# Kernel optimization log

Hardware: AMD Instinct MI355X
Metric: run time of the kernel (lower is better)

Reference implementation:

```python
import jax, jax.numpy as jnp
import numpy as np

DIM_IN = 1024
DIM_Q = 1024
DIM_K = 1024
DIM_V = 1024
HEADS = 16

def setup_inputs() -> dict:
    key = jax.random.key(0)
    ks = jax.random.split(key, 5)
    s = 1.0 / np.sqrt(DIM_IN)
    return {
        "x": jax.random.normal(ks[0], (2, 2048, DIM_IN), dtype=jnp.float32),
        "Wq": jax.random.uniform(ks[1], (DIM_IN, DIM_Q), jnp.float32, -s, s),
        "Wk": jax.random.uniform(ks[2], (DIM_IN, DIM_K), jnp.float32, -s, s),
        "Wv": jax.random.uniform(ks[3], (DIM_IN, DIM_V), jnp.float32, -s, s),
        "Wo": jax.random.uniform(ks[4], (DIM_V, DIM_V), jnp.float32, -1.0/np.sqrt(DIM_V), 1.0/np.sqrt(DIM_V)),
    }

def reference(x, Wq, Wk, Wv, Wo):
    B, S, _ = x.shape
    H = HEADS
    q = (x @ Wq).reshape(B, S, H, DIM_Q // H).transpose(0, 2, 1, 3)  # [B,H,S,dq]
    k = (x @ Wk).reshape(B, S, H, DIM_K // H).transpose(0, 2, 1, 3)
    v = (x @ Wv).reshape(B, S, H, DIM_V // H).transpose(0, 2, 1, 3)
    scores = jnp.einsum("bhsd,bhtd->bhst", q, k)  # no pre-softmax scaling (as in source)
    # NOTE: source divides by sqrt(dim_q) AFTER softmax — replicated faithfully.
    attn = jax.nn.softmax(scores, axis=-1) / jnp.sqrt(jnp.float32(DIM_Q))
    out = jnp.einsum("bhst,bhtd->bhsd", attn, v)  # [B,H,S,dv]
    out = out.transpose(0, 2, 1, 3).reshape(B, S, DIM_V)
    return out @ Wo
```

## Files before the change

### kernel.cpp

```cpp
#include <hip/hip_runtime.h>
#include <hip/hip_bf16.h>


typedef __attribute__((ext_vector_type(8))) short bf16x8;
typedef __attribute__((ext_vector_type(4))) short short4v;
typedef __attribute__((ext_vector_type(4))) float f32x4;
typedef __attribute__((ext_vector_type(2))) unsigned int u32x2;

typedef const __attribute__((address_space(1))) void gvoid_t;
typedef __attribute__((address_space(3))) void svoid_t;
#define GLDS16(g, l) \
  __builtin_amdgcn_global_load_lds((gvoid_t*)(g), (svoid_t*)(l), 16, 0, 0)

#define MFMA16(a, b, c) __builtin_amdgcn_mfma_f32_16x16x32_bf16((a), (b), (c), 0, 0, 0)

#if defined(__has_builtin)
#if __has_builtin(__builtin_amdgcn_exp2f)
#define EXP2(x) __builtin_amdgcn_exp2f(x)
#else
#define EXP2(x) exp2f(x)
#endif
#else
#define EXP2(x) exp2f(x)
#endif

#define LOG2E 1.4426950408889634f
#define NSHIFT 17.312340490667561f

static __device__ __forceinline__ short f2bf(float f) {
  __hip_bfloat16 h = __float2bfloat16(f);
  short s;
  __builtin_memcpy(&s, &h, 2);
  return s;
}

static __device__ __forceinline__ unsigned pack2bf(float lo, float hi) {
  float2 t; t.x = lo; t.y = hi;
  __hip_bfloat162 h2 = __float22bfloat162_rn(t);
  unsigned u;
  __builtin_memcpy(&u, &h2, 4);
  return u;
}

__global__ __launch_bounds__(256) void prep(const float* __restrict__ x,
                                            const float* __restrict__ Wq,
                                            const float* __restrict__ Wk,
                                            const float* __restrict__ Wv,
                                            const float* __restrict__ Wo,
                                            short* __restrict__ xb,
                                            short* __restrict__ wqkvt,
                                            short* __restrict__ wot) {
  __shared__ float tile[64][65];
  int bid = blockIdx.x;
  int tid = threadIdx.x;
  if (bid < 2048) {
    int i = bid * 256 + tid;
    const float4* p = (const float4*)(x + (size_t)i * 8);
    float4 a = p[0], b = p[1];
    bf16x8 o;
    o[0] = f2bf(a.x); o[1] = f2bf(a.y); o[2] = f2bf(a.z); o[3] = f2bf(a.w);
    o[4] = f2bf(b.x); o[5] = f2bf(b.y); o[6] = f2bf(b.z); o[7] = f2bf(b.w);
    *(bf16x8*)(xb + (size_t)i * 8) = o;
    return;
  }
  bid -= 2048;
  int mat = bid >> 8;
  int t = bid & 255;
  int tn = (t & 15) * 64;
  int tk = (t >> 4) * 64;
  const float* src = (mat == 0) ? Wq : (mat == 1) ? Wk : (mat == 2) ? Wv : Wo;
  short* dst = (mat < 3) ? (wqkvt + (size_t)mat * 1024 * 1024) : wot;

  int c4 = (tid & 15) * 4;
#pragma unroll
  for (int it = 0; it < 4; ++it) {
    int r = (tid >> 4) + it * 16;
    float4 v = *(const float4*)(src + (size_t)(tk + r) * 1024 + tn + c4);
    tile[r][c4 + 0] = v.x; tile[r][c4 + 1] = v.y;
    tile[r][c4 + 2] = v.z; tile[r][c4 + 3] = v.w;
  }
  __syncthreads();
  int n = tid >> 2;
  int kc = (tid & 3) * 16;
  bf16x8 o0, o1;
#pragma unroll
  for (int j = 0; j < 8; ++j) {
    o0[j] = f2bf(tile[kc + j][n]);
    o1[j] = f2bf(tile[kc + 8 + j][n]);
  }
  *(bf16x8*)(dst + (size_t)(tn + n) * 1024 + tk + kc) = o0;
  *(bf16x8*)(dst + (size_t)(tn + n) * 1024 + tk + kc + 8) = o1;
}

__global__ __launch_bounds__(512, 4) void gemm_qkv(const short* __restrict__ A,
                                                   const short* __restrict__ Bt,
                                                   short* __restrict__ qk,
                                                   short* __restrict__ vt) {
  constexpr int K = 1024;
  __shared__ short As[2][128 * 64];
  __shared__ short Bs[2][192 * 64];
  const int tid = threadIdx.x;
  const int lane = tid & 63;
  const int w = tid >> 6;
  const int lr = lane & 15, lg = lane >> 4;
  const int m0 = blockIdx.y * 128, n0 = blockIdx.x * 192;
  const int wm = (w >> 2) * 64, wn = (w & 3) * 48;

  auto stage = [&](int kt, int bb) {
#pragma unroll
    for (int it = 0; it < 2; ++it) {
      int id = it * 512 + tid;
      int row = id >> 3, c = id & 7;
      int sc = c ^ (row & 7);
      GLDS16(A + (size_t)(m0 + row) * K + kt + sc * 8, &As[bb][0] + id * 8);
    }
#pragma unroll
    for (int it = 0; it < 3; ++it) {
      int id = it * 512 + tid;
      int row = id >> 3, c = id & 7;
      int sc = c ^ (row & 7);
      GLDS16(Bt + (size_t)(n0 + row) * K + kt + sc * 8, &Bs[bb][0] + id * 8);
    }
  };

  f32x4 acc[4][3] = {};

  stage(0, 0);
  __syncthreads();

  int cur = 0;
  for (int kt = 0; kt < K; kt += 64) {
    if (kt + 64 < K) stage(kt + 64, cur ^ 1);
    const short* Ab = &As[cur][0];
    const short* Bb = &Bs[cur][0];
#pragma unroll
    for (int kk2 = 0; kk2 < 2; ++kk2) {
      int cw = kk2 * 4 + lg;
      bf16x8 bfr[3];
#pragma unroll
      for (int ni = 0; ni < 3; ++ni) {
        int row = wn + ni * 16 + lr;
        bfr[ni] = *(const bf16x8*)(Bb + row * 64 + ((cw ^ (row & 7)) * 8));
      }
      __builtin_amdgcn_s_setprio(1);
#pragma unroll
      for (int mi = 0; mi < 4; ++mi) {
        int row = wm + mi * 16 + lr;
        bf16x8 af = *(const bf16x8*)(Ab + row * 64 + ((cw ^ (row & 7)) * 8));
#pragma unroll
        for (int ni = 0; ni < 3; ++ni)
          acc[mi][ni] = MFMA16(af, bfr[ni], acc[mi][ni]);
      }
      __builtin_amdgcn_s_setprio(0);
    }
    __syncthreads();
    cur ^= 1;
  }

#pragma unroll
  for (int mi = 0; mi < 4; ++mi) {
#pragma unroll
    for (int ni = 0; ni < 3; ++ni) {
      int m = m0 + wm + mi * 16 + lg * 4;
      int n = n0 + wn + ni * 16 + lr;
      if (n < 2048) {
        float sc = (n < 1024) ? LOG2E : 1.0f;
#pragma unroll
        for (int r = 0; r < 4; ++r)
          qk[(size_t)(m + r) * 2048 + n] = f2bf(acc[mi][ni][r] * sc);
      } else {
        int nv = n - 2048;
        int vtrow = ((m >> 11) * 16 + (nv >> 6)) * 64 + (nv & 63);
        int scol = m & 2047;
        int psc = (scol & ~31) | ((scol & 0xC) << 1) | ((scol & 16) >> 2) |
                  (scol & 3);
        short4v pv;
#pragma unroll
        for (int r = 0; r < 4; ++r) pv[r] = f2bf(acc[mi][ni][r]);
        *(short4v*)(vt + (size_t)vtrow * 2048 + psc) = pv;
      }
    }
  }
}

__global__ __launch_bounds__(256) void gemm_out(const short* __restrict__ A,
                                                const short* __restrict__ Bt,
                                                float* __restrict__ C) {
  constexpr int K = 1024, N = 1024;
  __shared__ short As[2][128 * 64];
  __shared__ short Bs[2][64 * 64];
  const int tid = threadIdx.x;
  const int lane = tid & 63;
  const int w = tid >> 6;
  const int lr = lane & 15, lg = lane >> 4;
  const int m0 = blockIdx.y * 128, n0 = blockIdx.x * 64;
  const int wm = (w >> 1) * 64, wn = (w & 1) * 32;

  auto stage = [&](int kt, int bb) {
#pragma unroll
    for (int it = 0; it < 4; ++it) {
      int id = it * 256 + tid;
      int row = id >> 3, c = id & 7;
      int sc = c ^ (row & 7);
      GLDS16(A + (size_t)(m0 + row) * K + kt + sc * 8, &As[bb][0] + id * 8);
    }
#pragma unroll
    for (int it = 0; it < 2; ++it) {
      int id = it * 256 + tid;
      int row = id >> 3, c = id & 7;
      int sc = c ^ (row & 7);
      GLDS16(Bt + (size_t)(n0 + row) * K + kt + sc * 8, &Bs[bb][0] + id * 8);
    }
  };

  f32x4 acc[4][2] = {};

  stage(0, 0);
  __syncthreads();

  int cur = 0;
  for (int kt = 0; kt < K; kt += 64) {
    if (kt + 64 < K) stage(kt + 64, cur ^ 1);
    const short* Ab = &As[cur][0];
    const short* Bb = &Bs[cur][0];
#pragma unroll
    for (int kk2 = 0; kk2 < 2; ++kk2) {
      int cw = kk2 * 4 + lg;
      bf16x8 bfr[2];
#pragma unroll
      for (int ni = 0; ni < 2; ++ni) {
        int row = wn + ni * 16 + lr;
        bfr[ni] = *(const bf16x8*)(Bb + row * 64 + ((cw ^ (row & 7)) * 8));
      }
      __builtin_amdgcn_s_setprio(1);
#pragma unroll
      for (int mi = 0; mi < 4; ++mi) {
        int row = wm + mi * 16 + lr;
        bf16x8 af = *(const bf16x8*)(Ab + row * 64 + ((cw ^ (row & 7)) * 8));
#pragma unroll
        for (int ni = 0; ni < 2; ++ni)
          acc[mi][ni] = MFMA16(af, bfr[ni], acc[mi][ni]);
      }
      __builtin_amdgcn_s_setprio(0);
    }
    __syncthreads();
    cur ^= 1;
  }

#pragma unroll
  for (int mi = 0; mi < 4; ++mi) {
#pragma unroll
    for (int ni = 0; ni < 2; ++ni) {
      int m = m0 + wm + mi * 16 + lg * 4;
      int n = n0 + wn + ni * 16 + lr;
#pragma unroll
      for (int r = 0; r < 4; ++r) C[(size_t)(m + r) * N + n] = acc[mi][ni][r];
    }
  }
}

__global__ __launch_bounds__(512, 4) void attn_fwd(const short* __restrict__ qk,
                                                   const short* __restrict__ vt,
                                                   short* __restrict__ outb) {
  constexpr int S = 2048, LDQ = 2048;
  const int fid = blockIdx.x;
  const int xcd = fid & 7, j = fid >> 3;
  const int qt = j & 15;
  const int pair = xcd * 4 + (j >> 4);
  const int h = pair & 15, b = pair >> 4;

  const int tid = threadIdx.x, lane = tid & 63, w = tid >> 6;
  const int lr = lane & 15, lg = lane >> 4;
  const int s7 = lr & 7;
  const int qb = qt * 128 + w * 16;

  __shared__ short Ks[2][128][64];
  __shared__ short Vs[2][64][128];

  const short* base = qk + (size_t)b * S * LDQ + h * 64;
  const short* vbase = vt + (size_t)(b * 16 + h) * 64 * 2048;

  bf16x8 qA0 = *(const bf16x8*)(base + (size_t)(qb + lr) * LDQ + lg * 8);
  bf16x8 qA1 = *(const bf16x8*)(base + (size_t)(qb + lr) * LDQ + 32 + lg * 8);

  auto stage = [&](int kt, int bb) {
#pragma unroll
    for (int it = 0; it < 2; ++it) {
      int id = it * 512 + tid;
      {
        int row = id >> 3, c = id & 7;
        int sc = c ^ (row & 7);
        GLDS16(base + 1024 + (size_t)(kt + row) * LDQ + sc * 8,
               &Ks[bb][0][0] + id * 8);
      }
      {
        int row = id >> 4, c = id & 15;
        int sc = c ^ (row & 15);
        GLDS16(vbase + (size_t)row * 2048 + kt + sc * 8,
               &Vs[bb][0][0] + id * 8);
      }
    }
  };

  f32x4 oA[4] = {};
  float lA = 0.f;

  stage(0, 0);
  __syncthreads();

  int cur = 0;
  for (int kt = 0; kt < S; kt += 128) {
    if (kt + 128 < S) stage(kt + 128, cur ^ 1);

    const short* Kb = &Ks[cur][0][0];
    const short* Vb = &Vs[cur][0][0];

    f32x4 sA[8];
    __builtin_amdgcn_s_setprio(1);
#pragma unroll
    for (int kc = 0; kc < 8; ++kc) {
      int krow = kc * 16 + lr;
      bf16x8 kf0 = *(const bf16x8*)(Kb + krow * 64 + ((lg ^ s7) * 8));
      bf16x8 kf1 = *(const bf16x8*)(Kb + krow * 64 + (((4 + lg) ^ s7) * 8));
      f32x4 s = {-NSHIFT, -NSHIFT, -NSHIFT, -NSHIFT};
      s = MFMA16(kf0, qA0, s);
      s = MFMA16(kf1, qA1, s);
      sA[kc] = s;
    }
    __builtin_amdgcn_s_setprio(0);

    float ls = 0.f;
    u32x2 pkA[8];
#pragma unroll
    for (int kc = 0; kc < 8; ++kc) {
      float p0 = EXP2(sA[kc][0]);
      float p1 = EXP2(sA[kc][1]);
      float p2 = EXP2(sA[kc][2]);
      float p3 = EXP2(sA[kc][3]);
      ls += (p0 + p1) + (p2 + p3);
      pkA[kc][0] = pack2bf(p0, p1);
      pkA[kc][1] = pack2bf(p2, p3);
    }
    lA += ls;

    bf16x8 pA[4];
#pragma unroll
    for (int g = 0; g < 4; ++g) {
      unsigned wv[4] = {pkA[2 * g][0], pkA[2 * g][1], pkA[2 * g + 1][0],
                        pkA[2 * g + 1][1]};
      __builtin_memcpy(&pA[g], wv, 16);
    }

    __builtin_amdgcn_s_setprio(1);
#pragma unroll
    for (int nc = 0; nc < 4; ++nc) {
      const short* vb = Vb + (nc * 16 + lr) * 128;
#pragma unroll
      for (int g = 0; g < 4; ++g) {
        bf16x8 vf = *(const bf16x8*)(vb + (((4 * g + lg) ^ lr) * 8));
        oA[nc] = MFMA16(pA[g], vf, oA[nc]);
      }
    }
    __builtin_amdgcn_s_setprio(0);
    __syncthreads();
    cur ^= 1;
  }

  float ltA = lA + __shfl_xor(lA, 16);
  ltA += __shfl_xor(ltA, 32);
#pragma unroll
  for (int r = 0; r < 4; ++r) {
    float dA = 1.0f / (__shfl(ltA, 4 * lg + r) * 32.0f);
#pragma unroll
    for (int nc = 0; nc < 4; ++nc) {
      int col = h * 64 + nc * 16 + lr;
      outb[(size_t)(b * S + qb + 4 * lg + r) * 1024 + col] = f2bf(oA[nc][r] * dA);
    }
  }
}

extern "C" void kernel_launch(void* const* d_in, const int* in_sizes, int n_in,
                              void* d_out, int out_size, void* d_ws,
                              size_t ws_size, hipStream_t stream) {
  (void)in_sizes; (void)n_in; (void)out_size; (void)ws_size;
  const float* x = (const float*)d_in[0];
  const float* Wq = (const float*)d_in[1];
  const float* Wk = (const float*)d_in[2];
  const float* Wv = (const float*)d_in[3];
  const float* Wo = (const float*)d_in[4];

  char* p = (char*)d_ws;
  short* xb = (short*)p;      p += (size_t)4096 * 1024 * 2;
  short* wqkvt = (short*)p;   p += (size_t)3072 * 1024 * 2;
  short* wot = (short*)p;     p += (size_t)1024 * 1024 * 2;
  short* qk = (short*)p;      p += (size_t)4096 * 2048 * 2;
  short* vt = (short*)p;      p += (size_t)4096 * 1024 * 2;
  short* attno = (short*)p;   p += (size_t)4096 * 1024 * 2;

  prep<<<3072, 256, 0, stream>>>(x, Wq, Wk, Wv, Wo, xb, wqkvt, wot);
  gemm_qkv<<<dim3(16, 32), 512, 0, stream>>>(xb, wqkvt, qk, vt);
  attn_fwd<<<512, 512, 0, stream>>>(qk, vt, attno);
  gemm_out<<<dim3(16, 32), 256, 0, stream>>>(attno, wot, (float*)d_out);
}
```

Before: 107.8 us.

## Process two 16-row query tiles per wave in attention to reuse K/V tiles

Each wave in the attention kernel now handles 32 query rows instead of 16, so every K and V fragment read from shared memory feeds two MFMA chains. The query block per workgroup doubles to 256 rows, the grid halves to 256 blocks, and launch bounds drop to 2 blocks per SM. This halves LDS traffic and global K/V staging per unit of work, at the cost of more registers per thread, fewer resident waves, and only 256 workgroups on a chip with many CUs, which may underfill the device.

```diff
diff --git a/kernel.cpp b/kernel.cpp
--- a/kernel.cpp
+++ b/kernel.cpp
@@ -259,20 +259,20 @@
   }
 }
 
-__global__ __launch_bounds__(512, 4) void attn_fwd(const short* __restrict__ qk,
+__global__ __launch_bounds__(512, 2) void attn_fwd(const short* __restrict__ qk,
                                                    const short* __restrict__ vt,
                                                    short* __restrict__ outb) {
   constexpr int S = 2048, LDQ = 2048;
   const int fid = blockIdx.x;
   const int xcd = fid & 7, j = fid >> 3;
-  const int qt = j & 15;
-  const int pair = xcd * 4 + (j >> 4);
+  const int qt = j & 7;
+  const int pair = xcd * 4 + (j >> 3);
   const int h = pair & 15, b = pair >> 4;
 
   const int tid = threadIdx.x, lane = tid & 63, w = tid >> 6;
   const int lr = lane & 15, lg = lane >> 4;
   const int s7 = lr & 7;
-  const int qb = qt * 128 + w * 16;
+  const int qb = qt * 256 + w * 32;
 
   __shared__ short Ks[2][128][64];
   __shared__ short Vs[2][64][128];
@@ -282,6 +282,8 @@
 
   bf16x8 qA0 = *(const bf16x8*)(base + (size_t)(qb + lr) * LDQ + lg * 8);
   bf16x8 qA1 = *(const bf16x8*)(base + (size_t)(qb + lr) * LDQ + 32 + lg * 8);
+  bf16x8 qB0 = *(const bf16x8*)(base + (size_t)(qb + 16 + lr) * LDQ + lg * 8);
+  bf16x8 qB1 = *(const bf16x8*)(base + (size_t)(qb + 16 + lr) * LDQ + 32 + lg * 8);
 
   auto stage = [&](int kt, int bb) {
 #pragma unroll
@@ -302,8 +304,8 @@
     }
   };
 
-  f32x4 oA[4] = {};
-  float lA = 0.f;
+  f32x4 oA[4] = {}, oB[4] = {};
+  float lA = 0.f, lB = 0.f;
 
   stage(0, 0);
   __syncthreads();
@@ -315,7 +317,7 @@
     const short* Kb = &Ks[cur][0][0];
     const short* Vb = &Vs[cur][0][0];
 
-    f32x4 sA[8];
+    f32x4 sA[8], sB[8];
     __builtin_amdgcn_s_setprio(1);
 #pragma unroll
     for (int kc = 0; kc < 8; ++kc) {
@@ -326,29 +328,40 @@
       s = MFMA16(kf0, qA0, s);
       s = MFMA16(kf1, qA1, s);
       sA[kc] = s;
+      f32x4 t = {-NSHIFT, -NSHIFT, -NSHIFT, -NSHIFT};
+      t = MFMA16(kf0, qB0, t);
+      t = MFMA16(kf1, qB1, t);
+      sB[kc] = t;
     }
     __builtin_amdgcn_s_setprio(0);
 
-    float ls = 0.f;
-    u32x2 pkA[8];
+    float lsA = 0.f, lsB = 0.f;
+    unsigned pwA[4][4], pwB[4][4];
 #pragma unroll
     for (int kc = 0; kc < 8; ++kc) {
-      float p0 = EXP2(sA[kc][0]);
-      float p1 = EXP2(sA[kc][1]);
-      float p2 = EXP2(sA[kc][2]);
-      float p3 = EXP2(sA[kc][3]);
-      ls += (p0 + p1) + (p2 + p3);
-      pkA[kc][0] = pack2bf(p0, p1);
-      pkA[kc][1] = pack2bf(p2, p3);
-    }
-    lA += ls;
-
-    bf16x8 pA[4];
+      {
+        float p0 = EXP2(sA[kc][0]), p1 = EXP2(sA[kc][1]);
+        float p2 = EXP2(sA[kc][2]), p3 = EXP2(sA[kc][3]);
+        lsA += (p0 + p1) + (p2 + p3);
+        pwA[kc >> 1][(kc & 1) * 2 + 0] = pack2bf(p0, p1);
+        pwA[kc >> 1][(kc & 1) * 2 + 1] = pack2bf(p2, p3);
+      }
+      {
+        float p0 = EXP2(sB[kc][0]), p1 = EXP2(sB[kc][1]);
+        float p2 = EXP2(sB[kc][2]), p3 = EXP2(sB[kc][3]);
+        lsB += (p0 + p1) + (p2 + p3);
+        pwB[kc >> 1][(kc & 1) * 2 + 0] = pack2bf(p0, p1);
+        pwB[kc >> 1][(kc & 1) * 2 + 1] = pack2bf(p2, p3);
+      }
+    }
+    lA += lsA;
+    lB += lsB;
+
+    bf16x8 pA[4], pB[4];
 #pragma unroll
     for (int g = 0; g < 4; ++g) {
-      unsigned wv[4] = {pkA[2 * g][0], pkA[2 * g][1], pkA[2 * g + 1][0],
-                        pkA[2 * g + 1][1]};
-      __builtin_memcpy(&pA[g], wv, 16);
+      __builtin_memcpy(&pA[g], pwA[g], 16);
+      __builtin_memcpy(&pB[g], pwB[g], 16);
     }
 
     __builtin_amdgcn_s_setprio(1);
@@ -359,6 +372,7 @@
       for (int g = 0; g < 4; ++g) {
         bf16x8 vf = *(const bf16x8*)(vb + (((4 * g + lg) ^ lr) * 8));
         oA[nc] = MFMA16(pA[g], vf, oA[nc]);
+        oB[nc] = MFMA16(pB[g], vf, oB[nc]);
       }
     }
     __builtin_amdgcn_s_setprio(0);
@@ -368,13 +382,18 @@
 
   float ltA = lA + __shfl_xor(lA, 16);
   ltA += __shfl_xor(ltA, 32);
+  float ltB = lB + __shfl_xor(lB, 16);
+  ltB += __shfl_xor(ltB, 32);
 #pragma unroll
   for (int r = 0; r < 4; ++r) {
     float dA = 1.0f / (__shfl(ltA, 4 * lg + r) * 32.0f);
+    float dB = 1.0f / (__shfl(ltB, 4 * lg + r) * 32.0f);
 #pragma unroll
     for (int nc = 0; nc < 4; ++nc) {
       int col = h * 64 + nc * 16 + lr;
       outb[(size_t)(b * S + qb + 4 * lg + r) * 1024 + col] = f2bf(oA[nc][r] * dA);
+      outb[(size_t)(b * S + qb + 16 + 4 * lg + r) * 1024 + col] =
+          f2bf(oB[nc][r] * dB);
     }
   }
 }
@@ -399,6 +418,6 @@
 
   prep<<<3072, 256, 0, stream>>>(x, Wq, Wk, Wv, Wo, xb, wqkvt, wot);
   gemm_qkv<<<dim3(16, 32), 512, 0, stream>>>(xb, wqkvt, qk, vt);
-  attn_fwd<<<512, 512, 0, stream>>>(qk, vt, attno);
+  attn_fwd<<<256, 512, 0, stream>>>(qk, vt, attno);
   gemm_out<<<dim3(16, 32), 256, 0, stream>>>(attno, wot, (float*)d_out);
 }
```

New measurement: 111.8 us. 1.04x slower.
